# Optimization experiments

Hardware: AMD Instinct MI355X
Metric: run time of the kernel (lower is better)

Reference implementation:

```python
import jax, jax.numpy as jnp
import numpy as np

NUM_USERS, NUM_ITEMS, NUM_GROUPS = 100000, 50000, 20000
D = 64
B, M = 16384, 50


def setup_inputs() -> dict:
    key = jax.random.key(0)
    ks = jax.random.split(key, 16)
    inp = {
        "group_inputs": jax.random.randint(ks[0], (B,), 0, NUM_GROUPS),
        "item_inputs": jax.random.randint(ks[1], (B,), 0, NUM_ITEMS),
        "member_ids": jax.random.randint(ks[2], (B, M), 0, NUM_USERS),
        "member_lengths": jax.random.randint(ks[3], (B,), 0, M),
        # embedding tables (xavier-ish scale)
        "user_table": jax.random.normal(ks[4], (NUM_USERS, D), jnp.float32) * 0.05,
        "item_table": jax.random.normal(ks[5], (NUM_ITEMS, D), jnp.float32) * 0.05,
        "group_table": jax.random.normal(ks[6], (NUM_GROUPS, D), jnp.float32) * 0.05,
        # attention MLP: 2D -> 16 -> 1
        "att_w1": jax.random.normal(ks[7], (2 * D, 16), jnp.float32) * 0.1,
        "att_b1": jnp.zeros((16,), jnp.float32),
        "att_w2": jax.random.normal(ks[8], (16, 1), jnp.float32) * 0.1,
        "att_b2": jnp.zeros((1,), jnp.float32),
        # predict MLP: 3D -> 8 -> 1
        "pred_w1": jax.random.normal(ks[9], (3 * D, 8), jnp.float32) * 0.1,
        "pred_b1": jnp.zeros((8,), jnp.float32),
        "pred_w2": jax.random.normal(ks[10], (8, 1), jnp.float32) * 0.1,
        "pred_b2": jnp.zeros((1,), jnp.float32),
    }
    return inp


def reference(group_inputs, item_inputs, member_ids, member_lengths,
              user_table, item_table, group_table,
              att_w1, att_b1, att_w2, att_b2,
              pred_w1, pred_b1, pred_w2, pred_b2):
    # mask: at least one valid member per group
    mask = jnp.arange(M)[None, :] <= member_lengths[:, None]          # [B, M] bool
    mem_e = user_table[member_ids]                                    # [B, M, D]
    item_e = item_table[item_inputs]                                  # [B, D]

    # attention over members: concat(member, item) -> 16 -> 1
    gi = jnp.concatenate(
        [mem_e, jnp.broadcast_to(item_e[:, None, :], mem_e.shape)], axis=-1)  # [B, M, 2D]
    h = jax.nn.relu(jnp.einsum('bmk,kh->bmh', gi, att_w1) + att_b1)   # [B, M, 16]
    scores = (jnp.einsum('bmh,ho->bmo', h, att_w2) + att_b2)[..., 0]  # [B, M]
    scores = jnp.where(mask, scores, -jnp.inf)
    at_wt = jax.nn.softmax(scores, axis=-1)                           # [B, M]

    g_att = jnp.einsum('bm,bmd->bd', at_wt, mem_e)                    # [B, D]
    g = g_att + group_table[group_inputs]                             # [B, D]

    elem = g * item_e
    new_e = jnp.concatenate([elem, g, item_e], axis=-1)               # [B, 3D]
    ph = jax.nn.relu(new_e @ pred_w1 + pred_b1)                       # [B, 8]
    y = jax.nn.sigmoid(ph @ pred_w2 + pred_b2)                        # [B, 1]
    return y
```

## Files before the change

kernel.cpp:

```cpp
#include <hip/hip_runtime.h>
#include <math.h>

constexpr int MM = 50;
constexpr int DD = 64;
constexpr int HH = 16;
constexpr int PH = 8;
constexpr int WAVES_PER_BLOCK = 4;

__global__ __launch_bounds__(256) void precompute_kernel(
    const float* __restrict__ user_table,
    const float* __restrict__ item_table,
    const float* __restrict__ att_w1,
    const float* __restrict__ att_b1,
    float* __restrict__ U,
    float* __restrict__ I,
    int nU, int nI, int userBlocks)
{
    const bool isU = (int)blockIdx.x < userBlocks;
    const int row = isU ? ((int)blockIdx.x * 256 + (int)threadIdx.x)
                        : (((int)blockIdx.x - userBlocks) * 256 + (int)threadIdx.x);
    const int n = isU ? nU : nI;
    if (row >= n) return;

    const float* __restrict__ src = isU ? user_table : item_table;
    const float* __restrict__ w1  = isU ? att_w1 : (att_w1 + DD * HH);
    const float4* rp = (const float4*)(src + (size_t)row * DD);

    float acc[HH];
    #pragma unroll
    for (int j = 0; j < HH; ++j) acc[j] = isU ? 0.0f : att_b1[j];

    #pragma unroll 4
    for (int d4 = 0; d4 < DD / 4; ++d4) {
        const float4 x = rp[d4];
        const float* w = w1 + (size_t)(d4 * 4) * HH;
        #pragma unroll
        for (int j = 0; j < HH; ++j) {
            acc[j] = fmaf(x.x, w[0 * HH + j], acc[j]);
            acc[j] = fmaf(x.y, w[1 * HH + j], acc[j]);
            acc[j] = fmaf(x.z, w[2 * HH + j], acc[j]);
            acc[j] = fmaf(x.w, w[3 * HH + j], acc[j]);
        }
    }

    float4* o4 = (float4*)((isU ? U : I) + (size_t)row * HH);
    o4[0] = make_float4(acc[0],  acc[1],  acc[2],  acc[3]);
    o4[1] = make_float4(acc[4],  acc[5],  acc[6],  acc[7]);
    o4[2] = make_float4(acc[8],  acc[9],  acc[10], acc[11]);
    o4[3] = make_float4(acc[12], acc[13], acc[14], acc[15]);
}

__global__ __launch_bounds__(256) void agree_main(
    const int* __restrict__ group_inputs,
    const int* __restrict__ item_inputs,
    const int* __restrict__ member_ids,
    const int* __restrict__ member_lengths,
    const float* __restrict__ user_table,
    const float* __restrict__ item_table,
    const float* __restrict__ group_table,
    const float* __restrict__ att_w2,
    const float* __restrict__ att_b2,
    const float* __restrict__ pred_w1,
    const float* __restrict__ pred_b1,
    const float* __restrict__ pred_w2,
    const float* __restrict__ pred_b2,
    const float* __restrict__ U,
    const float* __restrict__ I,
    float* __restrict__ out,
    int B)
{
    __shared__ float2 lds_pair[WAVES_PER_BLOCK][MM];

    const int lane = threadIdx.x & 63;
    const int wave = threadIdx.x >> 6;
    const int b = blockIdx.x * WAVES_PER_BLOCK + wave;
    if (b >= B) return;

    const int my_m = (lane < MM) ? lane : (MM - 1);
    const int my_id = member_ids[b * MM + my_m];
    const int item_idx = item_inputs[b];

    const float4* up = (const float4*)(U + (size_t)my_id * HH);
    const float4 u0 = up[0], u1 = up[1], u2 = up[2], u3 = up[3];
    const float* ip = I + (size_t)item_idx * HH;

    float score = att_b2[0];
    {
        const float uu[HH] = { u0.x,u0.y,u0.z,u0.w, u1.x,u1.y,u1.z,u1.w,
                               u2.x,u2.y,u2.z,u2.w, u3.x,u3.y,u3.z,u3.w };
        #pragma unroll
        for (int j = 0; j < HH; ++j)
            score = fmaf(fmaxf(uu[j] + ip[j], 0.0f), att_w2[j], score);
    }

    const int len = member_lengths[b];
    const bool valid = (lane < MM) && (lane <= len);
    score = valid ? score : -INFINITY;

    float mx = score;
    #pragma unroll
    for (int off = 32; off > 0; off >>= 1) mx = fmaxf(mx, __shfl_xor(mx, off, 64));
    float e = valid ? __expf(score - mx) : 0.0f;
    float sum = e;
    #pragma unroll
    for (int off = 32; off > 0; off >>= 1) sum += __shfl_xor(sum, off, 64);
    if (lane < MM)
        lds_pair[wave][lane] = make_float2(e / sum, __int_as_float(my_id));
    __builtin_amdgcn_s_waitcnt(0);

    const float item_d = item_table[(size_t)item_idx * DD + lane];

    const int mcnt = (len < MM - 1 ? len : MM - 1) + 1;
    float g = 0.0f;
    int m = 0;
    for (; m + 4 <= mcnt; m += 4) {
        const float2 q0 = lds_pair[wave][m + 0];
        const float2 q1 = lds_pair[wave][m + 1];
        const float2 q2 = lds_pair[wave][m + 2];
        const float2 q3 = lds_pair[wave][m + 3];
        const float x0 = user_table[(size_t)__float_as_int(q0.y) * DD + lane];
        const float x1 = user_table[(size_t)__float_as_int(q1.y) * DD + lane];
        const float x2 = user_table[(size_t)__float_as_int(q2.y) * DD + lane];
        const float x3 = user_table[(size_t)__float_as_int(q3.y) * DD + lane];
        g = fmaf(q0.x, x0, g);
        g = fmaf(q1.x, x1, g);
        g = fmaf(q2.x, x2, g);
        g = fmaf(q3.x, x3, g);
    }
    for (; m < mcnt; ++m) {
        const float2 q = lds_pair[wave][m];
        g = fmaf(q.x, user_table[(size_t)__float_as_int(q.y) * DD + lane], g);
    }
    const int gid = group_inputs[b];
    g += group_table[(size_t)gid * DD + lane];

    const float elem = g * item_d;
    float p[PH];
    {
        const float* pa = pred_w1 + (size_t)lane * PH;
        const float* pb = pred_w1 + (size_t)(DD + lane) * PH;
        const float* pc = pred_w1 + (size_t)(2 * DD + lane) * PH;
        #pragma unroll
        for (int j = 0; j < PH; ++j)
            p[j] = fmaf(elem, pa[j], fmaf(g, pb[j], item_d * pc[j]));
    }
    #pragma unroll
    for (int off = 32; off > 0; off >>= 1) {
        #pragma unroll
        for (int j = 0; j < PH; ++j) p[j] += __shfl_xor(p[j], off, 64);
    }

    if (lane == 0) {
        float acc = pred_b2[0];
        #pragma unroll
        for (int j = 0; j < PH; ++j)
            acc = fmaf(fmaxf(p[j] + pred_b1[j], 0.0f), pred_w2[j], acc);
        out[b] = 1.0f / (1.0f + __expf(-acc));
    }
}

__global__ __launch_bounds__(256) void agree_fallback(
    const int* __restrict__ group_inputs,
    const int* __restrict__ item_inputs,
    const int* __restrict__ member_ids,
    const int* __restrict__ member_lengths,
    const float* __restrict__ user_table,
    const float* __restrict__ item_table,
    const float* __restrict__ group_table,
    const float* __restrict__ att_w1,
    const float* __restrict__ att_b1,
    const float* __restrict__ att_w2,
    const float* __restrict__ att_b2,
    const float* __restrict__ pred_w1,
    const float* __restrict__ pred_b1,
    const float* __restrict__ pred_w2,
    const float* __restrict__ pred_b2,
    float* __restrict__ out,
    int B)
{
    __shared__ float lds_wt[WAVES_PER_BLOCK][MM];
    __shared__ int   lds_id[WAVES_PER_BLOCK][MM];

    const int lane = threadIdx.x & 63;
    const int wave = threadIdx.x >> 6;
    const int b = blockIdx.x * WAVES_PER_BLOCK + wave;
    if (b >= B) return;

    const int my_m = (lane < MM) ? lane : (MM - 1);
    const int my_id = member_ids[b * MM + my_m];
    if (lane < MM) lds_id[wave][lane] = my_id;

    const int item_idx = item_inputs[b];
    const float item_d = item_table[(size_t)item_idx * DD + lane];

    float h[HH];
    {
        const float* w1row = att_w1 + (size_t)(DD + lane) * HH;
        #pragma unroll
        for (int j = 0; j < HH; ++j) h[j] = item_d * w1row[j];
        #pragma unroll
        for (int off = 32; off > 0; off >>= 1) {
            #pragma unroll
            for (int j = 0; j < HH; ++j) h[j] += __shfl_xor(h[j], off, 64);
        }
        #pragma unroll
        for (int j = 0; j < HH; ++j) h[j] += att_b1[j];
    }

    const float* myrow = user_table + (size_t)my_id * DD;
    #pragma unroll 4
    for (int d4 = 0; d4 < DD / 4; ++d4) {
        const float4 x = ((const float4*)myrow)[d4];
        const float* w1d = att_w1 + (size_t)(d4 * 4) * HH;
        #pragma unroll
        for (int j = 0; j < HH; ++j) {
            h[j] = fmaf(x.x, w1d[0 * HH + j], h[j]);
            h[j] = fmaf(x.y, w1d[1 * HH + j], h[j]);
            h[j] = fmaf(x.z, w1d[2 * HH + j], h[j]);
            h[j] = fmaf(x.w, w1d[3 * HH + j], h[j]);
        }
    }

    float score = att_b2[0];
    #pragma unroll
    for (int j = 0; j < HH; ++j) score = fmaf(fmaxf(h[j], 0.0f), att_w2[j], score);

    const int len = member_lengths[b];
    const bool valid = (lane < MM) && (lane <= len);
    score = valid ? score : -INFINITY;

    float mx = score;
    #pragma unroll
    for (int off = 32; off > 0; off >>= 1) mx = fmaxf(mx, __shfl_xor(mx, off, 64));
    float e = valid ? __expf(score - mx) : 0.0f;
    float sum = e;
    #pragma unroll
    for (int off = 32; off > 0; off >>= 1) sum += __shfl_xor(sum, off, 64);
    if (lane < MM) lds_wt[wave][lane] = e / sum;
    __builtin_amdgcn_s_waitcnt(0);

    const int mcnt = (len < MM - 1 ? len : MM - 1) + 1;
    float g = 0.0f;
    #pragma unroll 2
    for (int m = 0; m < mcnt; ++m) {
        const float wm  = lds_wt[wave][m];
        const int   idm = lds_id[wave][m];
        g = fmaf(wm, user_table[(size_t)idm * DD + lane], g);
    }
    const int gid = group_inputs[b];
    g += group_table[(size_t)gid * DD + lane];

    const float elem = g * item_d;
    float p[PH];
    {
        const float* pa = pred_w1 + (size_t)lane * PH;
        const float* pb = pred_w1 + (size_t)(DD + lane) * PH;
        const float* pc = pred_w1 + (size_t)(2 * DD + lane) * PH;
        #pragma unroll
        for (int j = 0; j < PH; ++j)
            p[j] = fmaf(elem, pa[j], fmaf(g, pb[j], item_d * pc[j]));
    }
    #pragma unroll
    for (int off = 32; off > 0; off >>= 1) {
        #pragma unroll
        for (int j = 0; j < PH; ++j) p[j] += __shfl_xor(p[j], off, 64);
    }

    if (lane == 0) {
        float acc = pred_b2[0];
        #pragma unroll
        for (int j = 0; j < PH; ++j)
            acc = fmaf(fmaxf(p[j] + pred_b1[j], 0.0f), pred_w2[j], acc);
        out[b] = 1.0f / (1.0f + __expf(-acc));
    }
}

extern "C" void kernel_launch(void* const* d_in, const int* in_sizes, int n_in,
                              void* d_out, int out_size, void* d_ws, size_t ws_size,
                              hipStream_t stream) {
    const int*   group_inputs   = (const int*)d_in[0];
    const int*   item_inputs    = (const int*)d_in[1];
    const int*   member_ids     = (const int*)d_in[2];
    const int*   member_lengths = (const int*)d_in[3];
    const float* user_table     = (const float*)d_in[4];
    const float* item_table     = (const float*)d_in[5];
    const float* group_table    = (const float*)d_in[6];
    const float* att_w1         = (const float*)d_in[7];
    const float* att_b1         = (const float*)d_in[8];
    const float* att_w2         = (const float*)d_in[9];
    const float* att_b2         = (const float*)d_in[10];
    const float* pred_w1        = (const float*)d_in[11];
    const float* pred_b1        = (const float*)d_in[12];
    const float* pred_w2        = (const float*)d_in[13];
    const float* pred_b2        = (const float*)d_in[14];
    float* out = (float*)d_out;

    const int B  = in_sizes[0];
    const int nU = in_sizes[4] / DD;
    const int nI = in_sizes[5] / DD;
    const size_t need = (size_t)(nU + nI) * HH * sizeof(float);
    const int blocks = (B + WAVES_PER_BLOCK - 1) / WAVES_PER_BLOCK;

    if (ws_size >= need) {
        float* U = (float*)d_ws;
        float* I = U + (size_t)nU * HH;
        const int userBlocks = (nU + 255) / 256;
        const int itemBlocks = (nI + 255) / 256;
        precompute_kernel<<<userBlocks + itemBlocks, 256, 0, stream>>>(
            user_table, item_table, att_w1, att_b1, U, I, nU, nI, userBlocks);
        agree_main<<<blocks, 256, 0, stream>>>(
            group_inputs, item_inputs, member_ids, member_lengths,
            user_table, item_table, group_table,
            att_w2, att_b2, pred_w1, pred_b1, pred_w2, pred_b2,
            U, I, out, B);
    } else {
        agree_fallback<<<blocks, 256, 0, stream>>>(
            group_inputs, item_inputs, member_ids, member_lengths,
            user_table, item_table, group_table,
            att_w1, att_b1, att_w2, att_b2,
            pred_w1, pred_b1, pred_w2, pred_b2,
            out, B);
    }
}
```

Baseline: 144.5 us.

## Precompute item projections per batch row and gather member rows with float4 lanes

The precompute kernel now projects only the B items actually referenced, storing them per batch row instead of for the whole item table, which cuts the precompute work for items from the 50000-row table down to B gathered rows. The main kernel drops the LDS staging of weights and ids and broadcasts them with wave shuffles. The member gather is reorganised so each 16-lane quarter reads a float4 slice of a different member row, four members per pass, followed by a cross-quarter shuffle reduction. The prediction MLP is reworked to match the float4 layout. The aim is fewer, wider gather instructions and less precompute traffic, at the cost of extra shuffles and an extra indirection in the precompute step.

```diff
diff --git a/kernel.cpp b/kernel.cpp
--- a/kernel.cpp
+++ b/kernel.cpp
@@ -10,25 +10,37 @@
 __global__ __launch_bounds__(256) void precompute_kernel(
     const float* __restrict__ user_table,
     const float* __restrict__ item_table,
+    const int*   __restrict__ item_inputs,
     const float* __restrict__ att_w1,
     const float* __restrict__ att_b1,
     float* __restrict__ U,
-    float* __restrict__ I,
-    int nU, int nI, int userBlocks)
+    float* __restrict__ Ib,
+    int nU, int B, int userBlocks)
 {
     const bool isU = (int)blockIdx.x < userBlocks;
-    const int row = isU ? ((int)blockIdx.x * 256 + (int)threadIdx.x)
-                        : (((int)blockIdx.x - userBlocks) * 256 + (int)threadIdx.x);
-    const int n = isU ? nU : nI;
-    if (row >= n) return;
-
-    const float* __restrict__ src = isU ? user_table : item_table;
-    const float* __restrict__ w1  = isU ? att_w1 : (att_w1 + DD * HH);
-    const float4* rp = (const float4*)(src + (size_t)row * DD);
-
+    const float4* rp;
+    const float*  w1;
+    float* dst;
     float acc[HH];
-    #pragma unroll
-    for (int j = 0; j < HH; ++j) acc[j] = isU ? 0.0f : att_b1[j];
+
+    if (isU) {
+        const int row = (int)blockIdx.x * 256 + (int)threadIdx.x;
+        if (row >= nU) return;
+        rp  = (const float4*)(user_table + (size_t)row * DD);
+        w1  = att_w1;
+        dst = U + (size_t)row * HH;
+        #pragma unroll
+        for (int j = 0; j < HH; ++j) acc[j] = 0.0f;
+    } else {
+        const int r = ((int)blockIdx.x - userBlocks) * 256 + (int)threadIdx.x;
+        if (r >= B) return;
+        const int item = item_inputs[r];
+        rp  = (const float4*)(item_table + (size_t)item * DD);
+        w1  = att_w1 + (size_t)DD * HH;
+        dst = Ib + (size_t)r * HH;
+        #pragma unroll
+        for (int j = 0; j < HH; ++j) acc[j] = att_b1[j];
+    }
 
     #pragma unroll 4
     for (int d4 = 0; d4 < DD / 4; ++d4) {
@@ -43,7 +55,7 @@
         }
     }
 
-    float4* o4 = (float4*)((isU ? U : I) + (size_t)row * HH);
+    float4* o4 = (float4*)dst;
     o4[0] = make_float4(acc[0],  acc[1],  acc[2],  acc[3]);
     o4[1] = make_float4(acc[4],  acc[5],  acc[6],  acc[7]);
     o4[2] = make_float4(acc[8],  acc[9],  acc[10], acc[11]);
@@ -65,24 +77,22 @@
     const float* __restrict__ pred_w2,
     const float* __restrict__ pred_b2,
     const float* __restrict__ U,
-    const float* __restrict__ I,
+    const float* __restrict__ Ib,
     float* __restrict__ out,
     int B)
 {
-    __shared__ float2 lds_pair[WAVES_PER_BLOCK][MM];
-
     const int lane = threadIdx.x & 63;
     const int wave = threadIdx.x >> 6;
     const int b = blockIdx.x * WAVES_PER_BLOCK + wave;
     if (b >= B) return;
 
-    const int my_m = (lane < MM) ? lane : (MM - 1);
+    const int my_m  = (lane < MM) ? lane : (MM - 1);
     const int my_id = member_ids[b * MM + my_m];
-    const int item_idx = item_inputs[b];
+    const int len   = member_lengths[b];
 
     const float4* up = (const float4*)(U + (size_t)my_id * HH);
     const float4 u0 = up[0], u1 = up[1], u2 = up[2], u3 = up[3];
-    const float* ip = I + (size_t)item_idx * HH;
+    const float* ib = Ib + (size_t)b * HH;
 
     float score = att_b2[0];
     {
@@ -90,62 +100,88 @@
                                u2.x,u2.y,u2.z,u2.w, u3.x,u3.y,u3.z,u3.w };
         #pragma unroll
         for (int j = 0; j < HH; ++j)
-            score = fmaf(fmaxf(uu[j] + ip[j], 0.0f), att_w2[j], score);
-    }
-
-    const int len = member_lengths[b];
+            score = fmaf(fmaxf(uu[j] + ib[j], 0.0f), att_w2[j], score);
+    }
+
     const bool valid = (lane < MM) && (lane <= len);
     score = valid ? score : -INFINITY;
 
     float mx = score;
     #pragma unroll
     for (int off = 32; off > 0; off >>= 1) mx = fmaxf(mx, __shfl_xor(mx, off, 64));
-    float e = valid ? __expf(score - mx) : 0.0f;
+    const float e = valid ? __expf(score - mx) : 0.0f;
     float sum = e;
     #pragma unroll
     for (int off = 32; off > 0; off >>= 1) sum += __shfl_xor(sum, off, 64);
-    if (lane < MM)
-        lds_pair[wave][lane] = make_float2(e / sum, __int_as_float(my_id));
-    __builtin_amdgcn_s_waitcnt(0);
-
-    const float item_d = item_table[(size_t)item_idx * DD + lane];
-
-    const int mcnt = (len < MM - 1 ? len : MM - 1) + 1;
-    float g = 0.0f;
-    int m = 0;
-    for (; m + 4 <= mcnt; m += 4) {
-        const float2 q0 = lds_pair[wave][m + 0];
-        const float2 q1 = lds_pair[wave][m + 1];
-        const float2 q2 = lds_pair[wave][m + 2];
-        const float2 q3 = lds_pair[wave][m + 3];
-        const float x0 = user_table[(size_t)__float_as_int(q0.y) * DD + lane];
-        const float x1 = user_table[(size_t)__float_as_int(q1.y) * DD + lane];
-        const float x2 = user_table[(size_t)__float_as_int(q2.y) * DD + lane];
-        const float x3 = user_table[(size_t)__float_as_int(q3.y) * DD + lane];
-        g = fmaf(q0.x, x0, g);
-        g = fmaf(q1.x, x1, g);
-        g = fmaf(q2.x, x2, g);
-        g = fmaf(q3.x, x3, g);
-    }
-    for (; m < mcnt; ++m) {
-        const float2 q = lds_pair[wave][m];
-        g = fmaf(q.x, user_table[(size_t)__float_as_int(q.y) * DD + lane], g);
-    }
-    const int gid = group_inputs[b];
-    g += group_table[(size_t)gid * DD + lane];
-
-    const float elem = g * item_d;
+    const float wnorm = e / sum;
+
+    const int d4  = lane & 15;
+    const int rep = lane >> 4;
+    const int mcnt   = (len < MM - 1 ? len : MM - 1) + 1;
+    const int passes = (mcnt + 3) >> 2;
+
+    float4 g4 = make_float4(0.f, 0.f, 0.f, 0.f);
+    int pass = 0;
+    for (; pass + 2 <= passes; pass += 2) {
+        const int m0 = pass * 4 + rep;
+        const int m1 = m0 + 4;
+        const float w0 = __shfl(wnorm, m0, 64);
+        const int   i0 = __shfl(my_id, m0, 64);
+        const float w1 = __shfl(wnorm, m1, 64);
+        const int   i1 = __shfl(my_id, m1, 64);
+        const float4 x0 = ((const float4*)(user_table + (size_t)i0 * DD))[d4];
+        const float4 x1 = ((const float4*)(user_table + (size_t)i1 * DD))[d4];
+        g4.x = fmaf(w0, x0.x, g4.x); g4.y = fmaf(w0, x0.y, g4.y);
+        g4.z = fmaf(w0, x0.z, g4.z); g4.w = fmaf(w0, x0.w, g4.w);
+        g4.x = fmaf(w1, x1.x, g4.x); g4.y = fmaf(w1, x1.y, g4.y);
+        g4.z = fmaf(w1, x1.z, g4.z); g4.w = fmaf(w1, x1.w, g4.w);
+    }
+    if (pass < passes) {
+        const int m0 = pass * 4 + rep;
+        const float w0 = __shfl(wnorm, m0, 64);
+        const int   i0 = __shfl(my_id, m0, 64);
+        const float4 x0 = ((const float4*)(user_table + (size_t)i0 * DD))[d4];
+        g4.x = fmaf(w0, x0.x, g4.x); g4.y = fmaf(w0, x0.y, g4.y);
+        g4.z = fmaf(w0, x0.z, g4.z); g4.w = fmaf(w0, x0.w, g4.w);
+    }
+    #pragma unroll
+    for (int off = 16; off <= 32; off <<= 1) {
+        g4.x += __shfl_xor(g4.x, off, 64);
+        g4.y += __shfl_xor(g4.y, off, 64);
+        g4.z += __shfl_xor(g4.z, off, 64);
+        g4.w += __shfl_xor(g4.w, off, 64);
+    }
+
+    const int gid      = group_inputs[b];
+    const int item_idx = item_inputs[b];
+    const float4 gr  = ((const float4*)(group_table + (size_t)gid * DD))[d4];
+    const float4 it4 = ((const float4*)(item_table + (size_t)item_idx * DD))[d4];
+    g4.x += gr.x; g4.y += gr.y; g4.z += gr.z; g4.w += gr.w;
+    const float4 e4 = make_float4(g4.x * it4.x, g4.y * it4.y,
+                                  g4.z * it4.z, g4.w * it4.w);
+
     float p[PH];
+    #pragma unroll
+    for (int j = 0; j < PH; ++j) p[j] = 0.0f;
     {
-        const float* pa = pred_w1 + (size_t)lane * PH;
-        const float* pb = pred_w1 + (size_t)(DD + lane) * PH;
-        const float* pc = pred_w1 + (size_t)(2 * DD + lane) * PH;
-        #pragma unroll
-        for (int j = 0; j < PH; ++j)
-            p[j] = fmaf(elem, pa[j], fmaf(g, pb[j], item_d * pc[j]));
-    }
-    #pragma unroll
-    for (int off = 32; off > 0; off >>= 1) {
+        const float* wa = pred_w1 + (size_t)(4 * d4) * PH;
+        const float* wb = pred_w1 + (size_t)(DD + 4 * d4) * PH;
+        const float* wc = pred_w1 + (size_t)(2 * DD + 4 * d4) * PH;
+        const float ev[4] = { e4.x, e4.y, e4.z, e4.w };
+        const float gv[4] = { g4.x, g4.y, g4.z, g4.w };
+        const float iv[4] = { it4.x, it4.y, it4.z, it4.w };
+        #pragma unroll
+        for (int k = 0; k < 4; ++k) {
+            #pragma unroll
+            for (int j = 0; j < PH; ++j) {
+                p[j] = fmaf(ev[k], wa[k * PH + j],
+                       fmaf(gv[k], wb[k * PH + j],
+                       fmaf(iv[k], wc[k * PH + j], p[j])));
+            }
+        }
+    }
+    #pragma unroll
+    for (int off = 1; off <= 8; off <<= 1) {
         #pragma unroll
         for (int j = 0; j < PH; ++j) p[j] += __shfl_xor(p[j], off, 64);
     }
@@ -243,9 +279,8 @@
     float g = 0.0f;
     #pragma unroll 2
     for (int m = 0; m < mcnt; ++m) {
-        const float wm  = lds_wt[wave][m];
-        const int   idm = lds_id[wave][m];
-        g = fmaf(wm, user_table[(size_t)idm * DD + lane], g);
+        g = fmaf(lds_wt[wave][m],
+                 user_table[(size_t)lds_id[wave][m] * DD + lane], g);
     }
     const int gid = group_inputs[b];
     g += group_table[(size_t)gid * DD + lane];
@@ -297,22 +332,22 @@
 
     const int B  = in_sizes[0];
     const int nU = in_sizes[4] / DD;
-    const int nI = in_sizes[5] / DD;
-    const size_t need = (size_t)(nU + nI) * HH * sizeof(float);
+    const size_t need = ((size_t)nU + (size_t)B) * HH * sizeof(float);
     const int blocks = (B + WAVES_PER_BLOCK - 1) / WAVES_PER_BLOCK;
 
     if (ws_size >= need) {
-        float* U = (float*)d_ws;
-        float* I = U + (size_t)nU * HH;
+        float* U  = (float*)d_ws;
+        float* Ib = U + (size_t)nU * HH;
         const int userBlocks = (nU + 255) / 256;
-        const int itemBlocks = (nI + 255) / 256;
+        const int itemBlocks = (B + 255) / 256;
         precompute_kernel<<<userBlocks + itemBlocks, 256, 0, stream>>>(
-            user_table, item_table, att_w1, att_b1, U, I, nU, nI, userBlocks);
+            user_table, item_table, item_inputs, att_w1, att_b1,
+            U, Ib, nU, B, userBlocks);
         agree_main<<<blocks, 256, 0, stream>>>(
             group_inputs, item_inputs, member_ids, member_lengths,
             user_table, item_table, group_table,
             att_w2, att_b2, pred_w1, pred_b1, pred_w2, pred_b2,
-            U, I, out, B);
+            U, Ib, out, B);
     } else {
         agree_fallback<<<blocks, 256, 0, stream>>>(
             group_inputs, item_inputs, member_ids, member_lengths,
```

New measurement: 174.7 us. +20.9%, slower.
